# Kernel optimization log

Measured on AMD Instinct MI355X. Metric: run time of the kernel, lower is better.

Reference implementation:

```python
import jax, jax.numpy as jnp
from jax import lax
import numpy as np

DIM = 384
HEADS = 8
SR = 2
B, D0, D1, D2 = 4, 16, 16, 16
N = 1 + D0 * D1 * D2


def setup_inputs() -> dict:
    key = jax.random.key(0)
    ks = jax.random.split(key, 8)
    s = 0.02
    return {
        "x": jax.random.normal(ks[0], (B, N, DIM), dtype=jnp.float32),
        "q_w": jax.random.normal(ks[1], (DIM, DIM), dtype=jnp.float32) * s,
        "kv_w": jax.random.normal(ks[2], (2 * DIM, DIM), dtype=jnp.float32) * s,
        "proj_w": jax.random.normal(ks[3], (DIM, DIM), dtype=jnp.float32) * s,
        "proj_b": jnp.zeros((DIM,), dtype=jnp.float32),
        "sr_w": jax.random.normal(ks[4], (DIM, 1, SR, SR, SR), dtype=jnp.float32) * s,  # depthwise (groups=dim)
        "sr_b": jnp.zeros((DIM,), dtype=jnp.float32),
        "ln_g": jnp.ones((DIM,), dtype=jnp.float32),
        "ln_b": jnp.zeros((DIM,), dtype=jnp.float32),
        "d0": D0, "d1": D1, "d2": D2,
    }


def reference(x, q_w, kv_w, proj_w, proj_b, sr_w, sr_b, ln_g, ln_b, d0, d1, d2):
    B_, N_, C = x.shape
    hd = C // HEADS
    scale = hd ** -0.5

    # q projection -> [B, H, N, hd]
    q = (x @ q_w.T).reshape(B_, N_, HEADS, hd).transpose(0, 2, 1, 3)

    # spatial reduction of patch tokens (keep CLS token)
    x_ = x[:, 1:].transpose(0, 2, 1).reshape(B_, C, d0, d1, d2)
    x_ = lax.conv_general_dilated(
        x_, sr_w, window_strides=(SR, SR, SR), padding="VALID",
        dimension_numbers=("NCDHW", "OIDHW", "NCDHW"), feature_group_count=C,
    ) + sr_b[None, :, None, None, None]
    x_ = x_.reshape(B_, C, -1).transpose(0, 2, 1)           # [B, M-1, C]
    x_ = jnp.concatenate([x[:, 0:1], x_], axis=1)            # [B, M, C]

    # LayerNorm (eps=1e-5)
    mu = jnp.mean(x_, axis=-1, keepdims=True)
    var = jnp.var(x_, axis=-1, keepdims=True)
    x_ = (x_ - mu) / jnp.sqrt(var + 1e-5) * ln_g + ln_b

    M = x_.shape[1]
    kv = (x_ @ kv_w.T).reshape(B_, M, 2, HEADS, hd).transpose(2, 0, 3, 1, 4)
    k, v = kv[0], kv[1]                                      # [B, H, M, hd]

    attn = jax.nn.softmax(jnp.einsum("bhnd,bhmd->bhnm", q, k) * scale, axis=-1)
    out = jnp.einsum("bhnm,bhmd->bhnd", attn, v)
    out = out.transpose(0, 2, 1, 3).reshape(B_, N_, C)
    return out @ proj_w.T + proj_b
```

## Files before the change

### kernel.cpp

```cpp
#include <hip/hip_runtime.h>

typedef unsigned short u16;
typedef unsigned int u32;
typedef __bf16 bf16x8 __attribute__((ext_vector_type(8)));
typedef float f32x4 __attribute__((ext_vector_type(4)));

#define NTOK 4097
#define MTOK 513
#define MPAD 544
#define KPAD 640
#define NPAD_Q 4224
#define ROWS_X 16512

__device__ __forceinline__ u16 f2bf(float f) {
  u32 u = __builtin_bit_cast(u32, f);
  u = u + 0x7FFFu + ((u >> 16) & 1u);
  return (u16)(u >> 16);
}
__device__ __forceinline__ u16 f2bf_fast(float f) {
  u32 u = __builtin_bit_cast(u32, f);
  return (u16)((u + 0x8000u) >> 16);
}

__device__ __forceinline__ void gld16(const u16* g, u16* l) {
  __builtin_amdgcn_global_load_lds((const __attribute__((address_space(1))) u32*)g,
                                   (__attribute__((address_space(3))) u32*)l, 16, 0, 0);
}

#define NQW  147456
#define NKVW 294912
#define NPW  147456
#define GQW  (NQW / 8)
#define GKVW (NKVW / 8)
#define GPW  (NPW / 8)
#define GW   (GQW + GKVW + GPW)
#define SRLN_BLOCKS (4 * MTOK)
#define CAST_BLOCKS 192

__global__ void pre_kernel(const float* __restrict__ x, const float* __restrict__ qw,
                           const float* __restrict__ kvw, const float* __restrict__ pw,
                           const float* __restrict__ srw, const float* __restrict__ srb,
                           const float* __restrict__ lng, const float* __restrict__ lnb,
                           u16* __restrict__ qwb, u16* __restrict__ kvwb, u16* __restrict__ pwb,
                           u16* __restrict__ xln) {
  if (blockIdx.x < SRLN_BLOCKS) {
    int c = threadIdx.x;
    int bm = blockIdx.x;
    int b = bm / MTOK, m = bm - b * MTOK;
    float v;
    if (m == 0) {
      v = x[(b * NTOK) * 384 + c];
    } else {
      int mo = m - 1;
      int oz = mo >> 6, oy = (mo >> 3) & 7, ox = mo & 7;
      float acc = srb[c];
#pragma unroll
      for (int dz = 0; dz < 2; dz++)
#pragma unroll
        for (int dy = 0; dy < 2; dy++)
#pragma unroll
          for (int dx = 0; dx < 2; dx++) {
            int tok = 1 + ((2 * oz + dz) * 256 + (2 * oy + dy) * 16 + (2 * ox + dx));
            acc += x[(b * NTOK + tok) * 384 + c] * srw[c * 8 + dz * 4 + dy * 2 + dx];
          }
      v = acc;
    }
    float s1 = v, s2 = v * v;
#pragma unroll
    for (int msk = 32; msk >= 1; msk >>= 1) {
      s1 += __shfl_xor(s1, msk);
      s2 += __shfl_xor(s2, msk);
    }
    __shared__ float r1[6], r2[6];
    int w = threadIdx.x >> 6, lane = threadIdx.x & 63;
    if (lane == 0) { r1[w] = s1; r2[w] = s2; }
    __syncthreads();
    float S1 = 0.f, S2 = 0.f;
#pragma unroll
    for (int i = 0; i < 6; i++) { S1 += r1[i]; S2 += r2[i]; }
    float mu = S1 * (1.0f / 384.0f);
    float var = S2 * (1.0f / 384.0f) - mu * mu;
    float y = (v - mu) * rsqrtf(var + 1e-5f) * lng[c] + lnb[c];
    xln[(b * MPAD + m) * 384 + c] = f2bf(y);
  } else {
    int idx = (blockIdx.x - SRLN_BLOCKS) * blockDim.x + threadIdx.x;
    int stride = (gridDim.x - SRLN_BLOCKS) * blockDim.x;
    for (int g = idx; g < GW; g += stride) {
      const float* s;
      u16* d;
      int off;
      if (g < GQW) { s = qw; d = qwb; off = g * 8; }
      else if (g < GQW + GKVW) { s = kvw; d = kvwb; off = (g - GQW) * 8; }
      else { s = pw; d = pwb; off = (g - GQW - GKVW) * 8; }
      float4 v0 = *(const float4*)(s + off);
      float4 v1 = *(const float4*)(s + off + 4);
      uint4 o;
      u16* p = (u16*)&o;
      p[0] = f2bf(v0.x); p[1] = f2bf(v0.y); p[2] = f2bf(v0.z); p[3] = f2bf(v0.w);
      p[4] = f2bf(v1.x); p[5] = f2bf(v1.y); p[6] = f2bf(v1.z); p[7] = f2bf(v1.w);
      *(uint4*)(d + off) = o;
    }
  }
}

__device__ __forceinline__ void gemm_core(u16* aLds, u16* bLds,
                                          const u16* __restrict__ A, const u16* __restrict__ W,
                                          int mode, size_t rbase, int c0,
                                          u16* __restrict__ o1, u16* __restrict__ o2,
                                          float* __restrict__ of, const float* __restrict__ bias) {
  int tid = threadIdx.x, w = tid >> 6, lane = tid & 63, q4 = lane >> 4, c16 = lane & 15;
  int wr = w >> 1, wc = w & 1;
  int x7 = c16 & 7;

  auto stageAB = [&](int kc, int buf) {
#pragma unroll
    for (int i = 0; i < 4; i++) {
      int s = (w * 4 + i) * 64 + lane;
      int row = s >> 3, chp = s & 7;
      int ch = chp ^ (row & 7);
      gld16(A + (rbase + row) * 384 + kc * 64 + ch * 8, &aLds[buf * 8192 + (w * 4 + i) * 512]);
    }
#pragma unroll
    for (int i = 0; i < 4; i++) {
      int s = (w * 4 + i) * 64 + lane;
      int row = s >> 3, chp = s & 7;
      int ch = chp ^ (row & 7);
      gld16(W + (size_t)(c0 + row) * 384 + kc * 64 + ch * 8, &bLds[buf * 8192 + (w * 4 + i) * 512]);
    }
  };
  stageAB(0, 0);
  __syncthreads();

  f32x4 acc[4][4];
#pragma unroll
  for (int mt = 0; mt < 4; mt++)
#pragma unroll
    for (int nt = 0; nt < 4; nt++) acc[mt][nt] = (f32x4){0, 0, 0, 0};

  for (int c = 0; c < 6; c++) {
    int cb = c & 1, nb = cb ^ 1;
    if (c < 5) stageAB(c + 1, nb);
#pragma unroll
    for (int ks = 0; ks < 2; ks++) {
      bf16x8 af[4], bf[4];
#pragma unroll
      for (int mt = 0; mt < 4; mt++)
        af[mt] = *(const bf16x8*)(&aLds[cb * 8192 + (wr * 64 + mt * 16 + c16) * 64 + ((ks * 4 + q4) ^ x7) * 8]);
#pragma unroll
      for (int nt = 0; nt < 4; nt++)
        bf[nt] = *(const bf16x8*)(&bLds[cb * 8192 + (wc * 64 + nt * 16 + c16) * 64 + ((ks * 4 + q4) ^ x7) * 8]);
#pragma unroll
      for (int mt = 0; mt < 4; mt++)
#pragma unroll
        for (int nt = 0; nt < 4; nt++)
          acc[mt][nt] = __builtin_amdgcn_mfma_f32_16x16x32_bf16(af[mt], bf[nt], acc[mt][nt], 0, 0, 0);
    }
    __syncthreads();
  }

#pragma unroll
  for (int mt = 0; mt < 4; mt++)
#pragma unroll
    for (int nt = 0; nt < 4; nt++) {
      int col = c0 + wc * 64 + nt * 16 + c16;
#pragma unroll
      for (int r = 0; r < 4; r++) {
        int R = (int)rbase + wr * 64 + mt * 16 + q4 * 4 + r;
        float val = acc[mt][nt][r];
        if (mode == 1) {
          int b = R / MPAD;
          int m = R - b * MPAD;
          if (col < 384) {
            int h = col / 48, d = col - h * 48;
            o1[((size_t)(b * 8 + h) * KPAD + m) * 64 + d] = f2bf(val);
          } else {
            int c2 = col - 384;
            int h = c2 / 48, d = c2 - h * 48;
            o2[((size_t)(b * 8 + h) * 48 + d) * KPAD + m] = f2bf(val);
          }
        } else {
          if (R < 4 * NTOK) of[(size_t)R * 384 + col] = val + bias[col];
        }
      }
    }
}

__device__ __forceinline__ void gemm_core_f32A(u16* aLds, u16* bLds,
                                               const float* __restrict__ X, const u16* __restrict__ W,
                                               size_t rbase, int c0, u16* __restrict__ o1) {
  int tid = threadIdx.x, w = tid >> 6, lane = tid & 63, q4 = lane >> 4, c16 = lane & 15;
  int wr = w >> 1, wc = w & 1;
  int x7 = c16 & 7;

  float4 ra[2][2];
  auto loadA2 = [&](int kc, int half) {
#pragma unroll
    for (int i = 0; i < 2; i++) {
      int idx2 = half * 2 + i;
      int s = (w * 4 + idx2) * 64 + lane;
      int row = s >> 3, chp = s & 7;
      int ch = chp ^ (row & 7);
      int ar = (int)rbase + row;
      if (ar > 16387) ar = 16387;
      const float* pa = X + (size_t)ar * 384 + kc * 64 + ch * 8;
      ra[i][0] = *(const float4*)pa;
      ra[i][1] = *(const float4*)(pa + 4);
    }
  };
  auto writeA2 = [&](int buf, int half) {
#pragma unroll
    for (int i = 0; i < 2; i++) {
      int idx2 = half * 2 + i;
      uint4 oa;
      u16* p = (u16*)&oa;
      p[0] = f2bf(ra[i][0].x); p[1] = f2bf(ra[i][0].y);
      p[2] = f2bf(ra[i][0].z); p[3] = f2bf(ra[i][0].w);
      p[4] = f2bf(ra[i][1].x); p[5] = f2bf(ra[i][1].y);
      p[6] = f2bf(ra[i][1].z); p[7] = f2bf(ra[i][1].w);
      *(uint4*)(&aLds[buf * 8192 + (w * 4 + idx2) * 512 + lane * 8]) = oa;
    }
  };
  auto stageB = [&](int kc, int buf) {
#pragma unroll
    for (int i = 0; i < 4; i++) {
      int s = (w * 4 + i) * 64 + lane;
      int row = s >> 3, chp = s & 7;
      int ch = chp ^ (row & 7);
      gld16(W + (size_t)(c0 + row) * 384 + kc * 64 + ch * 8, &bLds[buf * 8192 + (w * 4 + i) * 512]);
    }
  };

  loadA2(0, 0);
  stageB(0, 0);
  writeA2(0, 0);
  loadA2(0, 1);
  writeA2(0, 1);
  __syncthreads();

  f32x4 acc[4][4];
#pragma unroll
  for (int mt = 0; mt < 4; mt++)
#pragma unroll
    for (int nt = 0; nt < 4; nt++) acc[mt][nt] = (f32x4){0, 0, 0, 0};

  for (int c = 0; c < 6; c++) {
    int cb = c & 1, nb = cb ^ 1;
    if (c < 5) { loadA2(c + 1, 0); stageB(c + 1, nb); }
    {
      bf16x8 af[4], bf[4];
#pragma unroll
      for (int mt = 0; mt < 4; mt++)
        af[mt] = *(const bf16x8*)(&aLds[cb * 8192 + (wr * 64 + mt * 16 + c16) * 64 + ((0 + q4) ^ x7) * 8]);
#pragma unroll
      for (int nt = 0; nt < 4; nt++)
        bf[nt] = *(const bf16x8*)(&bLds[cb * 8192 + (wc * 64 + nt * 16 + c16) * 64 + ((0 + q4) ^ x7) * 8]);
#pragma unroll
      for (int mt = 0; mt < 4; mt++)
#pragma unroll
        for (int nt = 0; nt < 4; nt++)
          acc[mt][nt] = __builtin_amdgcn_mfma_f32_16x16x32_bf16(af[mt], bf[nt], acc[mt][nt], 0, 0, 0);
    }
    if (c < 5) { writeA2(nb, 0); loadA2(c + 1, 1); }
    {
      bf16x8 af[4], bf[4];
#pragma unroll
      for (int mt = 0; mt < 4; mt++)
        af[mt] = *(const bf16x8*)(&aLds[cb * 8192 + (wr * 64 + mt * 16 + c16) * 64 + ((4 + q4) ^ x7) * 8]);
#pragma unroll
      for (int nt = 0; nt < 4; nt++)
        bf[nt] = *(const bf16x8*)(&bLds[cb * 8192 + (wc * 64 + nt * 16 + c16) * 64 + ((4 + q4) ^ x7) * 8]);
#pragma unroll
      for (int mt = 0; mt < 4; mt++)
#pragma unroll
        for (int nt = 0; nt < 4; nt++)
          acc[mt][nt] = __builtin_amdgcn_mfma_f32_16x16x32_bf16(af[mt], bf[nt], acc[mt][nt], 0, 0, 0);
    }
    if (c < 5) writeA2(nb, 1);
    __syncthreads();
  }

#pragma unroll
  for (int mt = 0; mt < 4; mt++)
#pragma unroll
    for (int nt = 0; nt < 4; nt++) {
      int col = c0 + wc * 64 + nt * 16 + c16;
#pragma unroll
      for (int r = 0; r < 4; r++) {
        int R = (int)rbase + wr * 64 + mt * 16 + q4 * 4 + r;
        int b = R / NTOK;
        if (b >= 4) continue;
        int n = R - b * NTOK;
        int h = col / 48, d = col - h * 48;
        o1[((size_t)(b * 8 + h) * NPAD_Q + n) * 64 + d] =
            f2bf(acc[mt][nt][r] * 0.14433756729740643f);
      }
    }
}

__global__ __launch_bounds__(256) void gemm_qkv(const float* __restrict__ x, const u16* __restrict__ qwb,
                                                const u16* __restrict__ xlnb, const u16* __restrict__ kvwb,
                                                u16* __restrict__ qb, u16* __restrict__ kb2,
                                                u16* __restrict__ vtb) {
  __shared__ __align__(16) u16 aLds[2 * 128 * 64];
  __shared__ __align__(16) u16 bLds[2 * 128 * 64];
  int bx = blockIdx.x;
  if (bx < 387) {
    gemm_core_f32A(aLds, bLds, x, qwb, (size_t)(bx % 129) * 128, (bx / 129) * 128, qb);
  } else {
    int i = bx - 387;
    gemm_core(aLds, bLds, xlnb, kvwb, 1, (size_t)(i % 17) * 128, (i / 17) * 128,
              kb2, vtb, nullptr, nullptr);
  }
}

__global__ __launch_bounds__(256) void gemm_out(const u16* __restrict__ A, const u16* __restrict__ W,
                                                float* __restrict__ of, const float* __restrict__ bias) {
  __shared__ __align__(16) u16 aLds[2 * 128 * 64];
  __shared__ __align__(16) u16 bLds[2 * 128 * 64];
  gemm_core(aLds, bLds, A, W, 2, (size_t)blockIdx.x * 128, blockIdx.y * 128,
            nullptr, nullptr, of, bias);
}

__global__ __launch_bounds__(256, 4) void attn_kernel(const u16* __restrict__ qb,
                                                      const u16* __restrict__ kb,
                                                      const u16* __restrict__ vt,
                                                      u16* __restrict__ outb) {
  __shared__ __align__(16) u16 klds[2][64][64];
  __shared__ __align__(16) u16 vlds[2][48][64];
  __shared__ __align__(16) u16 plds[4][16][76];
  int tid = threadIdx.x, w = tid >> 6, lane = tid & 63, q4 = lane >> 4, c16 = lane & 15;
  int bh = blockIdx.x;
  int n0 = blockIdx.y * 128 + w * 32;
  int r7 = c16 & 7;

  const uint4* qp = (const uint4*)(qb + ((size_t)bh * NPAD_Q + n0 + c16) * 64);
  bf16x8 aq[2][2];
#pragma unroll
  for (int rg = 0; rg < 2; rg++) {
    aq[rg][0] = __builtin_bit_cast(bf16x8, qp[rg * 128 + q4]);
    aq[rg][1] = __builtin_bit_cast(bf16x8, qp[rg * 128 + 4 + q4]);
  }

  const u16* kbase = kb + (size_t)bh * KPAD * 64;
  const u16* vbase = vt + (size_t)bh * 48 * KPAD;

  auto stage = [&](int cn, int buf) {
#pragma unroll
    for (int i = 0; i < 2; i++) {
      int s = (w * 2 + i) * 64 + lane;
      int row = s >> 3, chp = s & 7;
      int ch = chp ^ (row & 7);
      gld16(kbase + (size_t)(cn * 64 + row) * 64 + ch * 8, &klds[buf][(w * 2 + i) * 8][0]);
    }
#pragma unroll
    for (int i = 0; i < 2; i++) {
      int blk = w * 2 + i;
      if (blk < 6) {
        int s = blk * 64 + lane;
        int row = s >> 3, chp = s & 7;
        int ch = chp ^ (row & 7);
        gld16(vbase + (size_t)row * KPAD + cn * 64 + ch * 8, &vlds[buf][blk * 8][0]);
      }
    }
  };

  stage(0, 0);
  __syncthreads();

  f32x4 o[2][3];
  float lsum[2][4];
#pragma unroll
  for (int rg = 0; rg < 2; rg++) {
#pragma unroll
    for (int nt = 0; nt < 3; nt++) o[rg][nt] = (f32x4){0, 0, 0, 0};
#pragma unroll
    for (int r = 0; r < 4; r++) lsum[rg][r] = 0.f;
  }

  for (int c = 0; c < 8; c++) {
    int cb = c & 1, nb = cb ^ 1;
    stage(c + 1, nb);

    f32x4 s[2][4];
#pragma unroll
    for (int rg = 0; rg < 2; rg++)
#pragma unroll
      for (int t = 0; t < 4; t++) s[rg][t] = (f32x4){0, 0, 0, 0};
#pragma unroll
    for (int t = 0; t < 4; t++) {
      const u16* krow = &klds[cb][t * 16 + c16][0];
      bf16x8 k0 = *(const bf16x8*)(krow + (q4 ^ r7) * 8);
      bf16x8 k1 = *(const bf16x8*)(krow + ((q4 ^ r7) ^ 4) * 8);
#pragma unroll
      for (int rg = 0; rg < 2; rg++) {
        s[rg][t] = __builtin_amdgcn_mfma_f32_16x16x32_bf16(aq[rg][0], k0, s[rg][t], 0, 0, 0);
        s[rg][t] = __builtin_amdgcn_mfma_f32_16x16x32_bf16(aq[rg][1], k1, s[rg][t], 0, 0, 0);
      }
    }
#pragma unroll
    for (int rg = 0; rg < 2; rg++)
#pragma unroll
      for (int t = 0; t < 4; t++)
#pragma unroll
        for (int r = 0; r < 4; r++) {
          float e = __expf(s[rg][t][r]);
          s[rg][t][r] = e;
          lsum[rg][r] += e;
        }
    bf16x8 afrag[2][2];
#pragma unroll
    for (int rg = 0; rg < 2; rg++) {
#pragma unroll
      for (int t = 0; t < 4; t++)
#pragma unroll
        for (int r = 0; r < 4; r++) plds[w][q4 * 4 + r][t * 16 + c16] = f2bf_fast(s[rg][t][r]);
#pragma unroll
      for (int kl = 0; kl < 2; kl++)
        afrag[rg][kl] = *(const bf16x8*)(&plds[w][c16][kl * 32 + q4 * 8]);
    }
#pragma unroll
    for (int kl = 0; kl < 2; kl++)
#pragma unroll
      for (int nt = 0; nt < 3; nt++) {
        const u16* vrow = &vlds[cb][nt * 16 + c16][0];
        bf16x8 bv = *(const bf16x8*)(vrow + ((kl * 4 + q4) ^ r7) * 8);
#pragma unroll
        for (int rg = 0; rg < 2; rg++)
          o[rg][nt] = __builtin_amdgcn_mfma_f32_16x16x32_bf16(afrag[rg][kl], bv, o[rg][nt], 0, 0, 0);
      }
    __syncthreads();
  }

  {
    f32x4 s4[2] = {{0, 0, 0, 0}, {0, 0, 0, 0}};
    const u16* krow = &klds[0][c16][0];
    bf16x8 k0 = *(const bf16x8*)(krow + (q4 ^ r7) * 8);
    bf16x8 k1 = *(const bf16x8*)(krow + ((q4 ^ r7) ^ 4) * 8);
#pragma unroll
    for (int rg = 0; rg < 2; rg++) {
      s4[rg] = __builtin_amdgcn_mfma_f32_16x16x32_bf16(aq[rg][0], k0, s4[rg], 0, 0, 0);
      s4[rg] = __builtin_amdgcn_mfma_f32_16x16x32_bf16(aq[rg][1], k1, s4[rg], 0, 0, 0);
    }
    bf16x8 afrag[2];
#pragma unroll
    for (int rg = 0; rg < 2; rg++) {
#pragma unroll
      for (int r = 0; r < 4; r++) {
        float e = (c16 == 0) ? __expf(s4[rg][r]) : 0.f;
        lsum[rg][r] += e;
        plds[w][q4 * 4 + r][c16] = f2bf_fast(e);
        plds[w][q4 * 4 + r][16 + c16] = 0;
      }
      afrag[rg] = *(const bf16x8*)(&plds[w][c16][q4 * 8]);
    }
#pragma unroll
    for (int nt = 0; nt < 3; nt++) {
      const u16* vrow = &vlds[0][nt * 16 + c16][0];
      bf16x8 bv = *(const bf16x8*)(vrow + (q4 ^ r7) * 8);
#pragma unroll
      for (int rg = 0; rg < 2; rg++)
        o[rg][nt] = __builtin_amdgcn_mfma_f32_16x16x32_bf16(afrag[rg], bv, o[rg][nt], 0, 0, 0);
    }
  }

  int b = bh >> 3, h = bh & 7;
#pragma unroll
  for (int rg = 0; rg < 2; rg++) {
    float inv[4];
#pragma unroll
    for (int r = 0; r < 4; r++) {
      float l = lsum[rg][r];
      l += __shfl_xor(l, 1);
      l += __shfl_xor(l, 2);
      l += __shfl_xor(l, 4);
      l += __shfl_xor(l, 8);
      inv[r] = 1.0f / l;
    }
#pragma unroll
    for (int nt = 0; nt < 3; nt++)
#pragma unroll
      for (int r = 0; r < 4; r++) {
        int n = n0 + rg * 16 + q4 * 4 + r;
        if (n < NTOK) outb[((size_t)(b * NTOK + n)) * 384 + h * 48 + nt * 16 + c16] = f2bf(o[rg][nt][r] * inv[r]);
      }
  }
}

extern "C" void kernel_launch(void* const* d_in, const int* in_sizes, int n_in,
                              void* d_out, int out_size, void* d_ws, size_t ws_size,
                              hipStream_t stream) {
  const float* x = (const float*)d_in[0];
  const float* q_w = (const float*)d_in[1];
  const float* kv_w = (const float*)d_in[2];
  const float* proj_w = (const float*)d_in[3];
  const float* proj_b = (const float*)d_in[4];
  const float* sr_w = (const float*)d_in[5];
  const float* sr_b = (const float*)d_in[6];
  const float* ln_g = (const float*)d_in[7];
  const float* ln_b = (const float*)d_in[8];
  float* out = (float*)d_out;

  u16* ws = (u16*)d_ws;
  u16* x_b = ws;
  u16* qw_b = x_b + (size_t)ROWS_X * 384;
  u16* kvw_b = qw_b + 147456;
  u16* pw_b = kvw_b + 294912;
  u16* q_b = pw_b + 147456;
  u16* xln_b = q_b + (size_t)32 * NPAD_Q * 64;
  u16* k_b = xln_b + (size_t)4 * MPAD * 384;
  u16* vt_b = k_b + (size_t)32 * KPAD * 64;
  u16* attn_b = x_b;


  pre_kernel<<<SRLN_BLOCKS + CAST_BLOCKS, 384, 0, stream>>>(x, q_w, kv_w, proj_w, sr_w, sr_b,
                                                            ln_g, ln_b, qw_b, kvw_b, pw_b, xln_b);
  gemm_qkv<<<489, 256, 0, stream>>>(x, qw_b, xln_b, kvw_b, q_b, k_b, vt_b);
  attn_kernel<<<dim3(32, 33), 256, 0, stream>>>(q_b, k_b, vt_b, attn_b);
  gemm_out<<<dim3(129, 3), 256, 0, stream>>>(attn_b, pw_b, out, proj_b);
}
```

Before: 177.3 us.

## Single-buffer GEMM LDS for higher occupancy and add MFMA priority hints in attention

Both GEMM kernels drop LDS double buffering and use a single 32KB stage, with load, sync, compute, sync per K chunk. Launch bounds of 3 blocks per CU let more workgroups hide latency in place of the software pipeline. The fp32-A path now prefetches the next chunk into registers while the current chunk computes. The attention kernel wraps its MFMA sections in s_setprio so waves doing matrix work get issue priority. The cost is less intra-block overlap of global loads and more barriers per chunk.

```diff
diff --git a/kernel.cpp b/kernel.cpp
--- a/kernel.cpp
+++ b/kernel.cpp
@@ -112,24 +112,22 @@
   int wr = w >> 1, wc = w & 1;
   int x7 = c16 & 7;
 
-  auto stageAB = [&](int kc, int buf) {
+  auto stageAB = [&](int kc) {
 #pragma unroll
     for (int i = 0; i < 4; i++) {
       int s = (w * 4 + i) * 64 + lane;
       int row = s >> 3, chp = s & 7;
       int ch = chp ^ (row & 7);
-      gld16(A + (rbase + row) * 384 + kc * 64 + ch * 8, &aLds[buf * 8192 + (w * 4 + i) * 512]);
+      gld16(A + (rbase + row) * 384 + kc * 64 + ch * 8, &aLds[(w * 4 + i) * 512]);
     }
 #pragma unroll
     for (int i = 0; i < 4; i++) {
       int s = (w * 4 + i) * 64 + lane;
       int row = s >> 3, chp = s & 7;
       int ch = chp ^ (row & 7);
-      gld16(W + (size_t)(c0 + row) * 384 + kc * 64 + ch * 8, &bLds[buf * 8192 + (w * 4 + i) * 512]);
+      gld16(W + (size_t)(c0 + row) * 384 + kc * 64 + ch * 8, &bLds[(w * 4 + i) * 512]);
     }
   };
-  stageAB(0, 0);
-  __syncthreads();
 
   f32x4 acc[4][4];
 #pragma unroll
@@ -138,24 +136,24 @@
     for (int nt = 0; nt < 4; nt++) acc[mt][nt] = (f32x4){0, 0, 0, 0};
 
   for (int c = 0; c < 6; c++) {
-    int cb = c & 1, nb = cb ^ 1;
-    if (c < 5) stageAB(c + 1, nb);
+    stageAB(c);
+    __syncthreads();
 #pragma unroll
     for (int ks = 0; ks < 2; ks++) {
       bf16x8 af[4], bf[4];
 #pragma unroll
       for (int mt = 0; mt < 4; mt++)
-        af[mt] = *(const bf16x8*)(&aLds[cb * 8192 + (wr * 64 + mt * 16 + c16) * 64 + ((ks * 4 + q4) ^ x7) * 8]);
+        af[mt] = *(const bf16x8*)(&aLds[(wr * 64 + mt * 16 + c16) * 64 + ((ks * 4 + q4) ^ x7) * 8]);
 #pragma unroll
       for (int nt = 0; nt < 4; nt++)
-        bf[nt] = *(const bf16x8*)(&bLds[cb * 8192 + (wc * 64 + nt * 16 + c16) * 64 + ((ks * 4 + q4) ^ x7) * 8]);
+        bf[nt] = *(const bf16x8*)(&bLds[(wc * 64 + nt * 16 + c16) * 64 + ((ks * 4 + q4) ^ x7) * 8]);
 #pragma unroll
       for (int mt = 0; mt < 4; mt++)
 #pragma unroll
         for (int nt = 0; nt < 4; nt++)
           acc[mt][nt] = __builtin_amdgcn_mfma_f32_16x16x32_bf16(af[mt], bf[nt], acc[mt][nt], 0, 0, 0);
     }
-    __syncthreads();
+    if (c < 5) __syncthreads();
   }
 
 #pragma unroll
@@ -192,12 +190,11 @@
   int wr = w >> 1, wc = w & 1;
   int x7 = c16 & 7;
 
-  float4 ra[2][2];
-  auto loadA2 = [&](int kc, int half) {
-#pragma unroll
-    for (int i = 0; i < 2; i++) {
-      int idx2 = half * 2 + i;
-      int s = (w * 4 + idx2) * 64 + lane;
+  float4 ra[4][2];
+  auto loadA = [&](int kc) {
+#pragma unroll
+    for (int i = 0; i < 4; i++) {
+      int s = (w * 4 + i) * 64 + lane;
       int row = s >> 3, chp = s & 7;
       int ch = chp ^ (row & 7);
       int ar = (int)rbase + row;
@@ -207,35 +204,29 @@
       ra[i][1] = *(const float4*)(pa + 4);
     }
   };
-  auto writeA2 = [&](int buf, int half) {
-#pragma unroll
-    for (int i = 0; i < 2; i++) {
-      int idx2 = half * 2 + i;
+  auto writeA = [&]() {
+#pragma unroll
+    for (int i = 0; i < 4; i++) {
       uint4 oa;
       u16* p = (u16*)&oa;
       p[0] = f2bf(ra[i][0].x); p[1] = f2bf(ra[i][0].y);
       p[2] = f2bf(ra[i][0].z); p[3] = f2bf(ra[i][0].w);
       p[4] = f2bf(ra[i][1].x); p[5] = f2bf(ra[i][1].y);
       p[6] = f2bf(ra[i][1].z); p[7] = f2bf(ra[i][1].w);
-      *(uint4*)(&aLds[buf * 8192 + (w * 4 + idx2) * 512 + lane * 8]) = oa;
+      *(uint4*)(&aLds[(w * 4 + i) * 512 + lane * 8]) = oa;
     }
   };
-  auto stageB = [&](int kc, int buf) {
+  auto stageB = [&](int kc) {
 #pragma unroll
     for (int i = 0; i < 4; i++) {
       int s = (w * 4 + i) * 64 + lane;
       int row = s >> 3, chp = s & 7;
       int ch = chp ^ (row & 7);
-      gld16(W + (size_t)(c0 + row) * 384 + kc * 64 + ch * 8, &bLds[buf * 8192 + (w * 4 + i) * 512]);
+      gld16(W + (size_t)(c0 + row) * 384 + kc * 64 + ch * 8, &bLds[(w * 4 + i) * 512]);
     }
   };
 
-  loadA2(0, 0);
-  stageB(0, 0);
-  writeA2(0, 0);
-  loadA2(0, 1);
-  writeA2(0, 1);
-  __syncthreads();
+  loadA(0);
 
   f32x4 acc[4][4];
 #pragma unroll
@@ -244,39 +235,26 @@
     for (int nt = 0; nt < 4; nt++) acc[mt][nt] = (f32x4){0, 0, 0, 0};
 
   for (int c = 0; c < 6; c++) {
-    int cb = c & 1, nb = cb ^ 1;
-    if (c < 5) { loadA2(c + 1, 0); stageB(c + 1, nb); }
-    {
+    writeA();
+    stageB(c);
+    __syncthreads();
+    if (c < 5) loadA(c + 1);
+#pragma unroll
+    for (int ks = 0; ks < 2; ks++) {
       bf16x8 af[4], bf[4];
 #pragma unroll
       for (int mt = 0; mt < 4; mt++)
-        af[mt] = *(const bf16x8*)(&aLds[cb * 8192 + (wr * 64 + mt * 16 + c16) * 64 + ((0 + q4) ^ x7) * 8]);
+        af[mt] = *(const bf16x8*)(&aLds[(wr * 64 + mt * 16 + c16) * 64 + ((ks * 4 + q4) ^ x7) * 8]);
 #pragma unroll
       for (int nt = 0; nt < 4; nt++)
-        bf[nt] = *(const bf16x8*)(&bLds[cb * 8192 + (wc * 64 + nt * 16 + c16) * 64 + ((0 + q4) ^ x7) * 8]);
+        bf[nt] = *(const bf16x8*)(&bLds[(wc * 64 + nt * 16 + c16) * 64 + ((ks * 4 + q4) ^ x7) * 8]);
 #pragma unroll
       for (int mt = 0; mt < 4; mt++)
 #pragma unroll
         for (int nt = 0; nt < 4; nt++)
           acc[mt][nt] = __builtin_amdgcn_mfma_f32_16x16x32_bf16(af[mt], bf[nt], acc[mt][nt], 0, 0, 0);
     }
-    if (c < 5) { writeA2(nb, 0); loadA2(c + 1, 1); }
-    {
-      bf16x8 af[4], bf[4];
-#pragma unroll
-      for (int mt = 0; mt < 4; mt++)
-        af[mt] = *(const bf16x8*)(&aLds[cb * 8192 + (wr * 64 + mt * 16 + c16) * 64 + ((4 + q4) ^ x7) * 8]);
-#pragma unroll
-      for (int nt = 0; nt < 4; nt++)
-        bf[nt] = *(const bf16x8*)(&bLds[cb * 8192 + (wc * 64 + nt * 16 + c16) * 64 + ((4 + q4) ^ x7) * 8]);
-#pragma unroll
-      for (int mt = 0; mt < 4; mt++)
-#pragma unroll
-        for (int nt = 0; nt < 4; nt++)
-          acc[mt][nt] = __builtin_amdgcn_mfma_f32_16x16x32_bf16(af[mt], bf[nt], acc[mt][nt], 0, 0, 0);
-    }
-    if (c < 5) writeA2(nb, 1);
-    __syncthreads();
+    if (c < 5) __syncthreads();
   }
 
 #pragma unroll
@@ -297,12 +275,12 @@
     }
 }
 
-__global__ __launch_bounds__(256) void gemm_qkv(const float* __restrict__ x, const u16* __restrict__ qwb,
-                                                const u16* __restrict__ xlnb, const u16* __restrict__ kvwb,
-                                                u16* __restrict__ qb, u16* __restrict__ kb2,
-                                                u16* __restrict__ vtb) {
-  __shared__ __align__(16) u16 aLds[2 * 128 * 64];
-  __shared__ __align__(16) u16 bLds[2 * 128 * 64];
+__global__ __launch_bounds__(256, 3) void gemm_qkv(const float* __restrict__ x, const u16* __restrict__ qwb,
+                                                   const u16* __restrict__ xlnb, const u16* __restrict__ kvwb,
+                                                   u16* __restrict__ qb, u16* __restrict__ kb2,
+                                                   u16* __restrict__ vtb) {
+  __shared__ __align__(16) u16 aLds[128 * 64];
+  __shared__ __align__(16) u16 bLds[128 * 64];
   int bx = blockIdx.x;
   if (bx < 387) {
     gemm_core_f32A(aLds, bLds, x, qwb, (size_t)(bx % 129) * 128, (bx / 129) * 128, qb);
@@ -313,10 +291,10 @@
   }
 }
 
-__global__ __launch_bounds__(256) void gemm_out(const u16* __restrict__ A, const u16* __restrict__ W,
-                                                float* __restrict__ of, const float* __restrict__ bias) {
-  __shared__ __align__(16) u16 aLds[2 * 128 * 64];
-  __shared__ __align__(16) u16 bLds[2 * 128 * 64];
+__global__ __launch_bounds__(256, 3) void gemm_out(const u16* __restrict__ A, const u16* __restrict__ W,
+                                                   float* __restrict__ of, const float* __restrict__ bias) {
+  __shared__ __align__(16) u16 aLds[128 * 64];
+  __shared__ __align__(16) u16 bLds[128 * 64];
   gemm_core(aLds, bLds, A, W, 2, (size_t)blockIdx.x * 128, blockIdx.y * 128,
             nullptr, nullptr, of, bias);
 }
@@ -386,6 +364,7 @@
     for (int rg = 0; rg < 2; rg++)
 #pragma unroll
       for (int t = 0; t < 4; t++) s[rg][t] = (f32x4){0, 0, 0, 0};
+    __builtin_amdgcn_s_setprio(1);
 #pragma unroll
     for (int t = 0; t < 4; t++) {
       const u16* krow = &klds[cb][t * 16 + c16][0];
@@ -397,6 +376,7 @@
         s[rg][t] = __builtin_amdgcn_mfma_f32_16x16x32_bf16(aq[rg][1], k1, s[rg][t], 0, 0, 0);
       }
     }
+    __builtin_amdgcn_s_setprio(0);
 #pragma unroll
     for (int rg = 0; rg < 2; rg++)
 #pragma unroll
@@ -418,6 +398,7 @@
       for (int kl = 0; kl < 2; kl++)
         afrag[rg][kl] = *(const bf16x8*)(&plds[w][c16][kl * 32 + q4 * 8]);
     }
+    __builtin_amdgcn_s_setprio(1);
 #pragma unroll
     for (int kl = 0; kl < 2; kl++)
 #pragma unroll
@@ -428,6 +409,7 @@
         for (int rg = 0; rg < 2; rg++)
           o[rg][nt] = __builtin_amdgcn_mfma_f32_16x16x32_bf16(afrag[rg][kl], bv, o[rg][nt], 0, 0, 0);
       }
+    __builtin_amdgcn_s_setprio(0);
     __syncthreads();
   }
 
```

Result: no change. 178.5 us (+0.7%).

## Fuse all four stages into one persistent kernel with grid barriers

Applied to the files above, without the earlier changes.

Replaces the four separate launches (pre-processing, QKV GEMM, attention, output GEMM) with a single persistent kernel of 448 blocks that loops over virtual block indices and separates stages with atomic-counter grid barriers. This is meant to remove kernel launch gaps and tail drain between stages. In exchange, each stage is limited to 448 resident blocks with shared LDS, 256-thread blocks for the LayerNorm step, and spin-wait barriers. It relies on all blocks being co-resident, and barrier reset through a magic word could race across repeated calls.

```diff
diff --git a/kernel.cpp b/kernel.cpp
--- a/kernel.cpp
+++ b/kernel.cpp
@@ -11,6 +11,9 @@
 #define KPAD 640
 #define NPAD_Q 4224
 #define ROWS_X 16512
+
+#define NBLK 448
+#define MAGIC 0x1234ABCDu
 
 __device__ __forceinline__ u16 f2bf(float f) {
   u32 u = __builtin_bit_cast(u32, f);
@@ -34,77 +37,43 @@
 #define GKVW (NKVW / 8)
 #define GPW  (NPW / 8)
 #define GW   (GQW + GKVW + GPW)
-#define SRLN_BLOCKS (4 * MTOK)
-#define CAST_BLOCKS 192
-
-__global__ void pre_kernel(const float* __restrict__ x, const float* __restrict__ qw,
-                           const float* __restrict__ kvw, const float* __restrict__ pw,
-                           const float* __restrict__ srw, const float* __restrict__ srb,
-                           const float* __restrict__ lng, const float* __restrict__ lnb,
-                           u16* __restrict__ qwb, u16* __restrict__ kvwb, u16* __restrict__ pwb,
-                           u16* __restrict__ xln) {
-  if (blockIdx.x < SRLN_BLOCKS) {
-    int c = threadIdx.x;
-    int bm = blockIdx.x;
-    int b = bm / MTOK, m = bm - b * MTOK;
-    float v;
-    if (m == 0) {
-      v = x[(b * NTOK) * 384 + c];
-    } else {
-      int mo = m - 1;
-      int oz = mo >> 6, oy = (mo >> 3) & 7, ox = mo & 7;
-      float acc = srb[c];
-#pragma unroll
-      for (int dz = 0; dz < 2; dz++)
-#pragma unroll
-        for (int dy = 0; dy < 2; dy++)
-#pragma unroll
-          for (int dx = 0; dx < 2; dx++) {
-            int tok = 1 + ((2 * oz + dz) * 256 + (2 * oy + dy) * 16 + (2 * ox + dx));
-            acc += x[(b * NTOK + tok) * 384 + c] * srw[c * 8 + dz * 4 + dy * 2 + dx];
-          }
-      v = acc;
-    }
-    float s1 = v, s2 = v * v;
-#pragma unroll
-    for (int msk = 32; msk >= 1; msk >>= 1) {
-      s1 += __shfl_xor(s1, msk);
-      s2 += __shfl_xor(s2, msk);
-    }
-    __shared__ float r1[6], r2[6];
-    int w = threadIdx.x >> 6, lane = threadIdx.x & 63;
-    if (lane == 0) { r1[w] = s1; r2[w] = s2; }
-    __syncthreads();
-    float S1 = 0.f, S2 = 0.f;
-#pragma unroll
-    for (int i = 0; i < 6; i++) { S1 += r1[i]; S2 += r2[i]; }
-    float mu = S1 * (1.0f / 384.0f);
-    float var = S2 * (1.0f / 384.0f) - mu * mu;
-    float y = (v - mu) * rsqrtf(var + 1e-5f) * lng[c] + lnb[c];
-    xln[(b * MPAD + m) * 384 + c] = f2bf(y);
-  } else {
-    int idx = (blockIdx.x - SRLN_BLOCKS) * blockDim.x + threadIdx.x;
-    int stride = (gridDim.x - SRLN_BLOCKS) * blockDim.x;
-    for (int g = idx; g < GW; g += stride) {
-      const float* s;
-      u16* d;
-      int off;
-      if (g < GQW) { s = qw; d = qwb; off = g * 8; }
-      else if (g < GQW + GKVW) { s = kvw; d = kvwb; off = (g - GQW) * 8; }
-      else { s = pw; d = pwb; off = (g - GQW - GKVW) * 8; }
-      float4 v0 = *(const float4*)(s + off);
-      float4 v1 = *(const float4*)(s + off + 4);
-      uint4 o;
-      u16* p = (u16*)&o;
-      p[0] = f2bf(v0.x); p[1] = f2bf(v0.y); p[2] = f2bf(v0.z); p[3] = f2bf(v0.w);
-      p[4] = f2bf(v1.x); p[5] = f2bf(v1.y); p[6] = f2bf(v1.z); p[7] = f2bf(v1.w);
-      *(uint4*)(d + off) = o;
-    }
-  }
+#define P0_SRLN (4 * MTOK)
+#define P0_N    (P0_SRLN + 288)
+#define P1_N    489
+#define P2_N    1056
+#define P3_N    387
+
+__device__ __forceinline__ void gbar(u32* c) {
+  __syncthreads();
+  if (threadIdx.x == 0) {
+    __threadfence();
+    atomicAdd(c, 1u);
+    while (__hip_atomic_load(c, __ATOMIC_ACQUIRE, __HIP_MEMORY_SCOPE_AGENT) < NBLK)
+      __builtin_amdgcn_s_sleep(2);
+  }
+  __syncthreads();
+}
+
+__device__ __forceinline__ float srln_val(const float* __restrict__ x, const float* __restrict__ srw,
+                                          const float* __restrict__ srb, int b, int m, int c) {
+  if (m == 0) return x[(b * NTOK) * 384 + c];
+  int mo = m - 1;
+  int oz = mo >> 6, oy = (mo >> 3) & 7, ox = mo & 7;
+  float acc = srb[c];
+#pragma unroll
+  for (int dz = 0; dz < 2; dz++)
+#pragma unroll
+    for (int dy = 0; dy < 2; dy++)
+#pragma unroll
+      for (int dx = 0; dx < 2; dx++) {
+        int tok = 1 + ((2 * oz + dz) * 256 + (2 * oy + dy) * 16 + (2 * ox + dx));
+        acc += x[(b * NTOK + tok) * 384 + c] * srw[c * 8 + dz * 4 + dy * 2 + dx];
+      }
+  return acc;
 }
 
 __device__ __forceinline__ void gemm_core(u16* aLds, u16* bLds,
-                                          const u16* __restrict__ A, const u16* __restrict__ W,
+                                          const u16* A, const u16* __restrict__ W,
                                           int mode, size_t rbase, int c0,
                                           u16* __restrict__ o1, u16* __restrict__ o2,
                                           float* __restrict__ of, const float* __restrict__ bias) {
@@ -297,41 +266,18 @@
     }
 }
 
-__global__ __launch_bounds__(256) void gemm_qkv(const float* __restrict__ x, const u16* __restrict__ qwb,
-                                                const u16* __restrict__ xlnb, const u16* __restrict__ kvwb,
-                                                u16* __restrict__ qb, u16* __restrict__ kb2,
-                                                u16* __restrict__ vtb) {
-  __shared__ __align__(16) u16 aLds[2 * 128 * 64];
-  __shared__ __align__(16) u16 bLds[2 * 128 * 64];
-  int bx = blockIdx.x;
-  if (bx < 387) {
-    gemm_core_f32A(aLds, bLds, x, qwb, (size_t)(bx % 129) * 128, (bx / 129) * 128, qb);
-  } else {
-    int i = bx - 387;
-    gemm_core(aLds, bLds, xlnb, kvwb, 1, (size_t)(i % 17) * 128, (i / 17) * 128,
-              kb2, vtb, nullptr, nullptr);
-  }
-}
-
-__global__ __launch_bounds__(256) void gemm_out(const u16* __restrict__ A, const u16* __restrict__ W,
-                                                float* __restrict__ of, const float* __restrict__ bias) {
-  __shared__ __align__(16) u16 aLds[2 * 128 * 64];
-  __shared__ __align__(16) u16 bLds[2 * 128 * 64];
-  gemm_core(aLds, bLds, A, W, 2, (size_t)blockIdx.x * 128, blockIdx.y * 128,
-            nullptr, nullptr, of, bias);
-}
-
-__global__ __launch_bounds__(256, 4) void attn_kernel(const u16* __restrict__ qb,
-                                                      const u16* __restrict__ kb,
-                                                      const u16* __restrict__ vt,
-                                                      u16* __restrict__ outb) {
-  __shared__ __align__(16) u16 klds[2][64][64];
-  __shared__ __align__(16) u16 vlds[2][48][64];
-  __shared__ __align__(16) u16 plds[4][16][76];
+__device__ __forceinline__ void attn_body(int vb, u16* smem,
+                                          const u16* __restrict__ qb, const u16* __restrict__ kb,
+                                          const u16* __restrict__ vt, u16* __restrict__ outb) {
+  u16 (*klds)[64][64] = (u16(*)[64][64])(smem);
+  u16 (*vlds)[48][64] = (u16(*)[48][64])(smem + 8192);
+  u16 (*plds)[16][76] = (u16(*)[16][76])(smem + 14336);
   int tid = threadIdx.x, w = tid >> 6, lane = tid & 63, q4 = lane >> 4, c16 = lane & 15;
-  int bh = blockIdx.x;
-  int n0 = blockIdx.y * 128 + w * 32;
+  int bh = vb & 31;
+  int n0 = (vb >> 5) * 128 + w * 32;
   int r7 = c16 & 7;
+
+  __syncthreads();
 
   const uint4* qp = (const uint4*)(qb + ((size_t)bh * NPAD_Q + n0 + c16) * 64);
   bf16x8 aq[2][2];
@@ -484,6 +430,93 @@
         if (n < NTOK) outb[((size_t)(b * NTOK + n)) * 384 + h * 48 + nt * 16 + c16] = f2bf(o[rg][nt][r] * inv[r]);
       }
   }
+}
+
+__global__ __launch_bounds__(256, 2) void mega_kernel(
+    const float* __restrict__ x, const float* __restrict__ qw, const float* __restrict__ kvw,
+    const float* __restrict__ pw, const float* __restrict__ pb,
+    const float* __restrict__ srw, const float* __restrict__ srb,
+    const float* __restrict__ lng, const float* __restrict__ lnb,
+    u16* __restrict__ qwb, u16* __restrict__ kvwb, u16* __restrict__ pwb,
+    u16* __restrict__ xln, u16* __restrict__ qb, u16* __restrict__ kb, u16* __restrict__ vtb,
+    u16* attnb, float* __restrict__ out, u32* bar) {
+  __shared__ __align__(16) u16 smem[32768];
+  int tid = threadIdx.x;
+
+  if (blockIdx.x == 0 && tid == 0) {
+    bar[1] = 0; bar[2] = 0; bar[3] = 0;
+    __threadfence();
+    __hip_atomic_store(&bar[0], MAGIC, __ATOMIC_RELEASE, __HIP_MEMORY_SCOPE_AGENT);
+  }
+  if (tid == 0) {
+    while (__hip_atomic_load(&bar[0], __ATOMIC_ACQUIRE, __HIP_MEMORY_SCOPE_AGENT) != MAGIC)
+      __builtin_amdgcn_s_sleep(2);
+  }
+  __syncthreads();
+
+  for (int vb = blockIdx.x; vb < P0_N; vb += NBLK) {
+    if (vb < P0_SRLN) {
+      int b = vb / MTOK, m = vb - b * MTOK;
+      float v0 = srln_val(x, srw, srb, b, m, tid);
+      bool has2 = tid < 128;
+      float v1 = has2 ? srln_val(x, srw, srb, b, m, tid + 256) : 0.f;
+      float s1 = v0 + v1, s2 = v0 * v0 + v1 * v1;
+#pragma unroll
+      for (int msk = 32; msk >= 1; msk >>= 1) {
+        s1 += __shfl_xor(s1, msk);
+        s2 += __shfl_xor(s2, msk);
+      }
+      float* r1 = (float*)smem;
+      float* r2 = r1 + 4;
+      int w = tid >> 6, lane = tid & 63;
+      if (lane == 0) { r1[w] = s1; r2[w] = s2; }
+      __syncthreads();
+      float S1 = r1[0] + r1[1] + r1[2] + r1[3];
+      float S2 = r2[0] + r2[1] + r2[2] + r2[3];
+      float mu = S1 * (1.0f / 384.0f);
+      float var = S2 * (1.0f / 384.0f) - mu * mu;
+      float rs = rsqrtf(var + 1e-5f);
+      size_t rowb = (size_t)(b * MPAD + m) * 384;
+      xln[rowb + tid] = f2bf((v0 - mu) * rs * lng[tid] + lnb[tid]);
+      if (has2) xln[rowb + tid + 256] = f2bf((v1 - mu) * rs * lng[tid + 256] + lnb[tid + 256]);
+      __syncthreads();
+    } else {
+      int g = (vb - P0_SRLN) * 256 + tid;
+      const float* s;
+      u16* d;
+      int off;
+      if (g < GQW) { s = qw; d = qwb; off = g * 8; }
+      else if (g < GQW + GKVW) { s = kvw; d = kvwb; off = (g - GQW) * 8; }
+      else { s = pw; d = pwb; off = (g - GQW - GKVW) * 8; }
+      float4 v0 = *(const float4*)(s + off);
+      float4 v1 = *(const float4*)(s + off + 4);
+      uint4 o;
+      u16* p = (u16*)&o;
+      p[0] = f2bf(v0.x); p[1] = f2bf(v0.y); p[2] = f2bf(v0.z); p[3] = f2bf(v0.w);
+      p[4] = f2bf(v1.x); p[5] = f2bf(v1.y); p[6] = f2bf(v1.z); p[7] = f2bf(v1.w);
+      *(uint4*)(d + off) = o;
+    }
+  }
+  gbar(bar + 1);
+
+  for (int vb = blockIdx.x; vb < P1_N; vb += NBLK) {
+    if (vb < 387) {
+      gemm_core_f32A(smem, smem + 16384, x, qwb, (size_t)(vb % 129) * 128, (vb / 129) * 128, qb);
+    } else {
+      int i = vb - 387;
+      gemm_core(smem, smem + 16384, xln, kvwb, 1, (size_t)(i % 17) * 128, (i / 17) * 128,
+                kb, vtb, nullptr, nullptr);
+    }
+  }
+  gbar(bar + 2);
+
+  for (int vb = blockIdx.x; vb < P2_N; vb += NBLK)
+    attn_body(vb, smem, qb, kb, vtb, attnb);
+  gbar(bar + 3);
+
+  for (int vb = blockIdx.x; vb < P3_N; vb += NBLK)
+    gemm_core(smem, smem + 16384, attnb, pwb, 2, (size_t)(vb % 129) * 128, (vb / 129) * 128,
+              nullptr, nullptr, out, pb);
 }
 
 extern "C" void kernel_launch(void* const* d_in, const int* in_sizes, int n_in,
@@ -510,11 +543,8 @@
   u16* k_b = xln_b + (size_t)4 * MPAD * 384;
   u16* vt_b = k_b + (size_t)32 * KPAD * 64;
   u16* attn_b = x_b;
-
-
-  pre_kernel<<<SRLN_BLOCKS + CAST_BLOCKS, 384, 0, stream>>>(x, q_w, kv_w, proj_w, sr_w, sr_b,
-                                                            ln_g, ln_b, qw_b, kvw_b, pw_b, xln_b);
-  gemm_qkv<<<489, 256, 0, stream>>>(x, qw_b, xln_b, kvw_b, q_b, k_b, vt_b);
-  attn_kernel<<<dim3(32, 33), 256, 0, stream>>>(q_b, k_b, vt_b, attn_b);
-  gemm_out<<<dim3(129, 3), 256, 0, stream>>>(attn_b, pw_b, out, proj_b);
-}
+  u32* bar = (u32*)(ws + (size_t)60 * 1024 * 1024);
+
+  mega_kernel<<<NBLK, 256, 0, stream>>>(x, q_w, kv_w, proj_w, proj_b, sr_w, sr_b, ln_g, ln_b,
+                                        qw_b, kvw_b, pw_b, xln_b, q_b, k_b, vt_b, attn_b, out, bar);
+}
```

New measurement: 455.7 us. +156.9%, slower.
